# Performance work log

Measured on AMD Instinct MI355X. Metric: run time of the kernel, lower is better.

Reference implementation:

```python
import jax, jax.numpy as jnp
import numpy as np

HIDDEN = 4096
N_Q_HEADS = 32
N_KV_HEADS = 8
HEAD_DIM = 128
V_HEAD_DIM = 128
WINDOW = 1024
ROPE_THETA = 1000000.0
SEQ = 2048


def setup_inputs() -> dict:
    key = jax.random.key(0)
    ks = jax.random.split(key, 7)
    s = 0.02
    return {
        "hidden_states": jax.random.normal(ks[0], (SEQ, HIDDEN), dtype=jnp.float32),
        "positions": jnp.arange(SEQ, dtype=jnp.int32),
        "wq": jax.random.normal(ks[1], (HIDDEN, N_Q_HEADS * HEAD_DIM), dtype=jnp.float32) * s,
        "wk": jax.random.normal(ks[2], (HIDDEN, N_KV_HEADS * HEAD_DIM), dtype=jnp.float32) * s,
        "wv": jax.random.normal(ks[3], (HIDDEN, N_KV_HEADS * V_HEAD_DIM), dtype=jnp.float32) * s,
        "wo": jax.random.normal(ks[4], (N_Q_HEADS * V_HEAD_DIM, HIDDEN), dtype=jnp.float32) * s,
        "sink": jax.random.normal(ks[5], (N_Q_HEADS,), dtype=jnp.float32),
    }


def _apply_rope_neox(x, positions):
    # x: [S, H, D]; rotate full head_dim in neox (half-split) style
    d = x.shape[-1]
    inv_freq = 1.0 / (ROPE_THETA ** (jnp.arange(0, d, 2, dtype=jnp.float32) / d))
    freqs = positions.astype(jnp.float32)[:, None] * inv_freq[None, :]  # [S, D/2]
    cos = jnp.cos(freqs)[:, None, :]  # [S, 1, D/2]
    sin = jnp.sin(freqs)[:, None, :]
    x1, x2 = x[..., : d // 2], x[..., d // 2 :]
    return jnp.concatenate([x1 * cos - x2 * sin, x2 * cos + x1 * sin], axis=-1)


def reference(hidden_states, positions, wq, wk, wv, wo, sink):
    S = hidden_states.shape[0]
    scaling = HEAD_DIM ** -0.5
    q = (hidden_states @ wq).reshape(S, N_Q_HEADS, HEAD_DIM)
    k = (hidden_states @ wk).reshape(S, N_KV_HEADS, HEAD_DIM)
    v = (hidden_states @ wv).reshape(S, N_KV_HEADS, V_HEAD_DIM)

    q = _apply_rope_neox(q, positions)
    k = _apply_rope_neox(k, positions)

    groups = N_Q_HEADS // N_KV_HEADS
    k_rep = jnp.repeat(k, groups, axis=1)  # [S, Hq, D]
    v_rep = jnp.repeat(v, groups, axis=1)

    # [Hq, S(query), S(key)] attention scores
    scores = jnp.einsum("qhd,khd->hqk", q, k_rep) * scaling

    # causal + sliding-window mask: key j visible iff j <= i and i - j < WINDOW
    i = positions[:, None].astype(jnp.int32)
    j = positions[None, :].astype(jnp.int32)
    mask = (j <= i) & (i - j < WINDOW)  # [S, S]
    neg = jnp.finfo(scores.dtype).min
    scores = jnp.where(mask[None, :, :], scores, neg)

    # softmax with per-head attention sink logit in the denominator
    sink_l = sink[:, None, None]  # [Hq, 1, 1]
    m = jnp.maximum(scores.max(axis=-1, keepdims=True), sink_l)
    w = jnp.exp(scores - m)
    denom = w.sum(axis=-1, keepdims=True) + jnp.exp(sink_l - m)
    probs = w / denom

    attn = jnp.einsum("hqk,khd->qhd", probs, v_rep).reshape(S, N_Q_HEADS * V_HEAD_DIM)
    return attn @ wo
```

## Files before the change

kernel.cpp:

```cpp
#include <hip/hip_runtime.h>
#include <cstdint>
#include <cstddef>

typedef uint16_t u16;
typedef __bf16 bf16x8 __attribute__((ext_vector_type(8)));
typedef float f32x4 __attribute__((ext_vector_type(4)));
typedef u16 u16x8 __attribute__((ext_vector_type(8)));


__device__ __forceinline__ u16 f2bf(float f) {
    union { float f; uint32_t i; } v; v.f = f;
    uint32_t b = v.i;
    return (u16)((b + 0x7FFFu + ((b >> 16) & 1u)) >> 16);
}
__device__ __forceinline__ float bf2f(u16 u) {
    union { uint32_t i; float f; } v; v.i = ((uint32_t)u) << 16; return v.f;
}
__device__ __forceinline__ float nanfix(float x, float repl) {
    return (x == x && fabsf(x) < 1e30f) ? x : repl;
}
__device__ __forceinline__ void async16(const u16* g, u16* l) {
    __builtin_amdgcn_global_load_lds(
        (const __attribute__((address_space(1))) uint32_t*)g,
        (__attribute__((address_space(3))) uint32_t*)l, 16, 0, 0);
}

template<int N> __device__ __forceinline__ void waitvm() {
    static_assert(N >= 0 && N <= 14, "vmcnt range");
    if constexpr (N == 0)  asm volatile("s_waitcnt vmcnt(0)" ::: "memory");
    else if constexpr (N == 1)  asm volatile("s_waitcnt vmcnt(1)" ::: "memory");
    else if constexpr (N == 2)  asm volatile("s_waitcnt vmcnt(2)" ::: "memory");
    else if constexpr (N == 3)  asm volatile("s_waitcnt vmcnt(3)" ::: "memory");
    else if constexpr (N == 4)  asm volatile("s_waitcnt vmcnt(4)" ::: "memory");
    else if constexpr (N == 5)  asm volatile("s_waitcnt vmcnt(5)" ::: "memory");
    else if constexpr (N == 6)  asm volatile("s_waitcnt vmcnt(6)" ::: "memory");
    else if constexpr (N == 7)  asm volatile("s_waitcnt vmcnt(7)" ::: "memory");
    else if constexpr (N == 8)  asm volatile("s_waitcnt vmcnt(8)" ::: "memory");
    else if constexpr (N == 9)  asm volatile("s_waitcnt vmcnt(9)" ::: "memory");
    else if constexpr (N == 10) asm volatile("s_waitcnt vmcnt(10)" ::: "memory");
    else if constexpr (N == 11) asm volatile("s_waitcnt vmcnt(11)" ::: "memory");
    else if constexpr (N == 12) asm volatile("s_waitcnt vmcnt(12)" ::: "memory");
    else if constexpr (N == 13) asm volatile("s_waitcnt vmcnt(13)" ::: "memory");
    else                        asm volatile("s_waitcnt vmcnt(14)" ::: "memory");
}

__global__ void cvt_k(const float* __restrict__ in, u16* __restrict__ out) {
    const size_t i = ((size_t)blockIdx.x * 256 + threadIdx.x) * 8;
    const f32x4 a = *(const f32x4*)&in[i], b = *(const f32x4*)&in[i + 4];
    u16x8 s;
    #pragma unroll
    for (int e = 0; e < 4; e++) { s[e] = f2bf(a[e]); s[4 + e] = f2bf(b[e]); }
    *(u16x8*)&out[i] = s;
}

__global__ void cvtT_k(const float* __restrict__ in, u16* __restrict__ out,
                       int R, int C) {
    __shared__ float tile[64][65];
    const int bx = blockIdx.x * 64, by = blockIdx.y * 64;
    const int tid = threadIdx.x;
    const int lc = (tid & 15) * 4, lrw = tid >> 4;
    #pragma unroll
    for (int i = 0; i < 4; i++) {
        const f32x4 v = *(const f32x4*)&in[(size_t)(by + lrw + i * 16) * C + bx + lc];
        tile[lrw + i * 16][lc]     = v[0];
        tile[lrw + i * 16][lc + 1] = v[1];
        tile[lrw + i * 16][lc + 2] = v[2];
        tile[lrw + i * 16][lc + 3] = v[3];
    }
    __syncthreads();
    #pragma unroll
    for (int p = 0; p < 2; p++) {
        const int c = (tid >> 3) + p * 32, r0 = (tid & 7) * 8;
        u16x8 s;
        #pragma unroll
        for (int e = 0; e < 8; e++) s[e] = f2bf(tile[r0 + e][c]);
        *(u16x8*)&out[(size_t)(bx + c) * R + by + r0] = s;
    }
}


#define SB(g, kk, dst) async16(Bb + (size_t)((g) * 64 + rg) * 4096 + (kk) + sc, \
                               (dst) + ((g) * 64 + wave * 8) * 64)
#define SA(g, kk, dst) async16(Ab + (size_t)((g) * 32 + aro) * 4096 + (kk) + sc, \
                               (dst) + ((g) * 32 + wbA) * 64)

#define LOADA4(PH) do {                                                         \
    _Pragma("unroll")                                                           \
    for (int f = 0; f < 4; f++) {                                               \
        const int row = wr * 128 + ((PH) * 4 + f) * 16 + lr;                    \
        _Pragma("unroll")                                                       \
        for (int ks = 0; ks < 2; ks++)                                          \
            a[f][ks] = *(const bf16x8*)&Ac[row * 64 + (((ks * 4 + qd) ^ (row & 7)) * 8)]; \
    }                                                                           \
} while (0)

#define MFMAP4(PH) do {                                                         \
    __builtin_amdgcn_s_setprio(1);                                              \
    _Pragma("unroll")                                                           \
    for (int f = 0; f < 4; f++)                                                 \
        _Pragma("unroll")                                                       \
        for (int nn = 0; nn < NF; nn++)                                         \
            _Pragma("unroll")                                                   \
            for (int ks = 0; ks < 2; ks++)                                      \
                acc[(PH) * 4 + f][nn] = __builtin_amdgcn_mfma_f32_16x16x32_bf16(\
                    a[f][ks], b[nn][ks], acc[(PH) * 4 + f][nn], 0, 0, 0);       \
    __builtin_amdgcn_s_setprio(0);                                              \
} while (0)

#define PHASE_SYNC() do {                                                       \
    __builtin_amdgcn_s_barrier();                                               \
    asm volatile("s_waitcnt lgkmcnt(0)" ::: "memory");                          \
    __builtin_amdgcn_sched_barrier(0);                                          \
} while (0)

#define PHASE_END() do {                                                        \
    __builtin_amdgcn_s_barrier();                                               \
    __builtin_amdgcn_sched_barrier(0);                                          \
} while (0)

template<int NF, int ISS>
__device__ __forceinline__ void tile_body(
    const u16* __restrict__ Ab, const u16* __restrict__ Bb,
    const u16* Ac, const u16* Bc, u16* An, u16* Bn, int k1,
    int wave, int lr, int qd, int wr, int wc,
    int rg, int sc, int aro, int wbA, f32x4 (&acc)[8][NF])
{
    bf16x8 b[NF][2];
    bf16x8 a[4][2];

    #pragma unroll
    for (int nn = 0; nn < NF; nn++)
        #pragma unroll
        for (int ks = 0; ks < 2; ks++) {
            const int row = wc * (16 * NF) + nn * 16 + lr;
            b[nn][ks] = *(const bf16x8*)&Bc[row * 64 + (((ks * 4 + qd) ^ (row & 7)) * 8)];
        }
    LOADA4(0);
    if constexpr (ISS) {
        #pragma unroll
        for (int g = 0; g < NF; g++) SB(g, k1, Bn);
        SA(0, k1, An); SA(1, k1, An); SA(2, k1, An); SA(3, k1, An);
    }
    PHASE_SYNC();
    MFMAP4(0);
    waitvm<ISS ? NF + 4 : 0>();
    PHASE_END();
    LOADA4(1);
    PHASE_SYNC();
    MFMAP4(1);
    if constexpr (ISS) waitvm<2>();
    PHASE_END();
}

template<int NF, int MODE>
__global__ __launch_bounds__(512, 2) void gemm256(
    const u16* __restrict__ A, const u16* __restrict__ BT,
    u16* __restrict__ qk, u16* __restrict__ vT, float* __restrict__ Cf)
{
    alignas(16) __shared__ u16 As[2][256 * 64];
    alignas(16) __shared__ u16 Bs[2][NF * 64 * 64];

    const int tid = threadIdx.x;
    const int wave = tid >> 6, lane = tid & 63;
    const int lr = lane & 15, qd = lane >> 4;
    const int wr = wave >> 2, wc = wave & 3;

    const int x = blockIdx.x & 7, bi = blockIdx.x >> 3;
    const int m0 = ((x & 1) * 4 + (bi & 3)) * 256;
    const int n0 = ((x >> 1) * 8 + (bi >> 2)) * (NF * 64);

    const u16* __restrict__ Ab = A + (size_t)m0 * 4096;
    const u16* __restrict__ Bb = BT + (size_t)n0 * 4096;

    const int rg = tid >> 3;
    const int sc = ((tid & 7) ^ (rg & 7)) * 8;
    const int aro = (rg < 32) ? rg : (96 + rg);
    const int wbA = (wave < 4) ? wave * 8 : (96 + wave * 8);

    f32x4 acc[8][NF];
    #pragma unroll
    for (int i = 0; i < 8; i++)
        #pragma unroll
        for (int j = 0; j < NF; j++) acc[i][j] = (f32x4){0.f, 0.f, 0.f, 0.f};

    #pragma unroll
    for (int g = 0; g < NF; g++) SB(g, 0, &Bs[0][0]);
    SA(0, 0, &As[0][0]); SA(1, 0, &As[0][0]); SA(2, 0, &As[0][0]); SA(3, 0, &As[0][0]);
    waitvm<2>();
    __builtin_amdgcn_s_barrier();
    __builtin_amdgcn_sched_barrier(0);

    for (int t = 0; t < 63; ++t) {
        const bool odd = t & 1;
        tile_body<NF, 1>(Ab, Bb,
                         odd ? &As[1][0] : &As[0][0], odd ? &Bs[1][0] : &Bs[0][0],
                         odd ? &As[0][0] : &As[1][0], odd ? &Bs[0][0] : &Bs[1][0],
                         (t + 1) * 64, wave, lr, qd, wr, wc, rg, sc, aro, wbA, acc);
    }
    tile_body<NF, 0>(Ab, Bb, &As[1][0], &Bs[1][0], &As[0][0], &Bs[0][0], 0,
                     wave, lr, qd, wr, wc, rg, sc, aro, wbA, acc);

    #pragma unroll
    for (int i = 0; i < 8; i++)
        #pragma unroll
        for (int j = 0; j < NF; j++) {
            const int col = n0 + wc * (16 * NF) + j * 16 + lr;
            #pragma unroll
            for (int r = 0; r < 4; r++) {
                const int row = m0 + wr * 128 + i * 16 + qd * 4 + r;
                if constexpr (MODE == 0) {
                    const u16 val = f2bf(nanfix(acc[i][j][r], 1000.0f));
                    if (col < 5120) qk[(size_t)row * 5120 + col] = val;
                    else            vT[(size_t)(col - 5120) * 2048 + row] = val;
                } else {
                    Cf[(size_t)row * 4096 + col] = nanfix(acc[i][j][r], 30000.0f);
                }
            }
        }
}

#undef SB
#undef SA
#undef LOADA4
#undef MFMAP4
#undef PHASE_SYNC
#undef PHASE_END

__global__ void rope_k(u16* __restrict__ qk, const int* __restrict__ positions) {
    const int s = blockIdx.x;
    const int h = blockIdx.y * 4 + (threadIdx.x >> 6);
    const int t = threadIdx.x & 63;
    u16* base = qk + (size_t)s * 5120 + ((h < 32) ? h * 128 : 4096 + (h - 32) * 128);
    const float pos = (float)positions[s];
    const float freq = pos * exp2f(-(float)t * (19.931568569324174f / 64.f));
    const float c = cosf(freq), sn = sinf(freq);
    const float x1 = bf2f(base[t]), x2 = bf2f(base[t + 64]);
    base[t]      = f2bf(x1 * c - x2 * sn);
    base[t + 64] = f2bf(x2 * c + x1 * sn);
}

__global__ __launch_bounds__(256) void attn_k(
    const u16* __restrict__ qk, const u16* __restrict__ vT,
    const float* __restrict__ sink, u16* __restrict__ out)
{
    alignas(16) __shared__ u16 Ks[64 * 128];
    alignas(16) __shared__ u16 VsT[128 * 72];
    alignas(16) __shared__ u16 Ps[4][16 * 72];

    const int h = blockIdx.y, hk = h >> 2;
    const int q0 = blockIdx.x * 64;
    const int tid = threadIdx.x, wave = tid >> 6, lane = tid & 63;
    const int lr = lane & 15, qd = lane >> 4;
    const float scaling = 0.08838834764831845f;

    bf16x8 aq[4];
    #pragma unroll
    for (int kc = 0; kc < 4; kc++)
        aq[kc] = *(const bf16x8*)&qk[(size_t)(q0 + wave * 16 + lr) * 5120 + h * 128 + kc * 32 + qd * 8];

    const float sinkv = sink[h];
    float m_run[4], l_run[4];
    #pragma unroll
    for (int r = 0; r < 4; r++) { m_run[r] = sinkv; l_run[r] = 0.f; }
    f32x4 acc_o[8];
    #pragma unroll
    for (int i = 0; i < 8; i++) acc_o[i] = (f32x4){0.f, 0.f, 0.f, 0.f};

    const int jlo = (q0 - 1023) > 0 ? (q0 - 1023) : 0;
    const int t0 = jlo >> 6, t1 = q0 >> 6;

    for (int kt = t0; kt <= t1; kt++) {
        const int j0 = kt * 64;
        __syncthreads();
        #pragma unroll
        for (int p = 0; p < 4; p++) {
            const int idx = p * 256 + tid;
            const int r = idx >> 4, cs = idx & 15, c = cs ^ (r & 15);
            async16(&qk[(size_t)(j0 + r) * 5120 + 4096 + hk * 128 + c * 8],
                    Ks + (p * 256 + wave * 64) * 8);
        }
        #pragma unroll
        for (int p = 0; p < 4; p++) {
            const int idx = p * 256 + tid;
            const int vd = idx >> 3, sc2 = (idx & 7) * 8;
            const u16x8 v = *(const u16x8*)&vT[(size_t)(hk * 128 + vd) * 2048 + j0 + sc2];
            *(u16x8*)&VsT[vd * 72 + sc2] = v;
        }
        __syncthreads();

        float sv[4][4];
        #pragma unroll
        for (int nt = 0; nt < 4; nt++) {
            f32x4 s = (f32x4){0.f, 0.f, 0.f, 0.f};
            #pragma unroll
            for (int kc = 0; kc < 4; kc++) {
                const int krow = nt * 16 + lr;
                const bf16x8 bk = *(const bf16x8*)&Ks[(krow * 16 + ((kc * 4 + qd) ^ lr)) * 8];
                s = __builtin_amdgcn_mfma_f32_16x16x32_bf16(aq[kc], bk, s, 0, 0, 0);
            }
            #pragma unroll
            for (int r = 0; r < 4; r++) sv[nt][r] = s[r];
        }

        float rmax[4] = {-1e30f, -1e30f, -1e30f, -1e30f};
        #pragma unroll
        for (int nt = 0; nt < 4; nt++) {
            const int kpos = j0 + nt * 16 + lr;
            #pragma unroll
            for (int r = 0; r < 4; r++) {
                const int qpos = q0 + wave * 16 + qd * 4 + r;
                const bool ok = (kpos <= qpos) && (qpos - kpos < 1024);
                const float x = ok ? sv[nt][r] * scaling : -1e30f;
                sv[nt][r] = x;
                rmax[r] = fmaxf(rmax[r], x);
            }
        }
        #pragma unroll
        for (int off = 1; off < 16; off <<= 1)
            #pragma unroll
            for (int r = 0; r < 4; r++)
                rmax[r] = fmaxf(rmax[r], __shfl_xor(rmax[r], off, 64));

        float alpha[4], rsum[4];
        #pragma unroll
        for (int r = 0; r < 4; r++) {
            const float mnew = fmaxf(m_run[r], rmax[r]);
            alpha[r] = __expf(m_run[r] - mnew);
            m_run[r] = mnew;
            rsum[r] = 0.f;
        }
        #pragma unroll
        for (int nt = 0; nt < 4; nt++)
            #pragma unroll
            for (int r = 0; r < 4; r++) {
                const float p = __expf(sv[nt][r] - m_run[r]);
                sv[nt][r] = p;
                rsum[r] += p;
            }
        #pragma unroll
        for (int off = 1; off < 16; off <<= 1)
            #pragma unroll
            for (int r = 0; r < 4; r++)
                rsum[r] += __shfl_xor(rsum[r], off, 64);
        #pragma unroll
        for (int r = 0; r < 4; r++)
            l_run[r] = l_run[r] * alpha[r] + rsum[r];

        #pragma unroll
        for (int nt = 0; nt < 4; nt++)
            #pragma unroll
            for (int r = 0; r < 4; r++)
                Ps[wave][(qd * 4 + r) * 72 + nt * 16 + lr] = f2bf(sv[nt][r]);

        #pragma unroll
        for (int i = 0; i < 8; i++)
            #pragma unroll
            for (int r = 0; r < 4; r++) acc_o[i][r] *= alpha[r];

        asm volatile("s_waitcnt lgkmcnt(0)" ::: "memory");
        __builtin_amdgcn_sched_barrier(0);

        bf16x8 pa[2];
        #pragma unroll
        for (int kc = 0; kc < 2; kc++)
            pa[kc] = *(const bf16x8*)&Ps[wave][lr * 72 + kc * 32 + qd * 8];

        #pragma unroll
        for (int nt = 0; nt < 8; nt++)
            #pragma unroll
            for (int kc = 0; kc < 2; kc++) {
                const bf16x8 bv = *(const bf16x8*)&VsT[(nt * 16 + lr) * 72 + kc * 32 + qd * 8];
                acc_o[nt] = __builtin_amdgcn_mfma_f32_16x16x32_bf16(pa[kc], bv, acc_o[nt], 0, 0, 0);
            }
    }

    float invd[4];
    #pragma unroll
    for (int r = 0; r < 4; r++)
        invd[r] = 1.f / (l_run[r] + __expf(sinkv - m_run[r]));
    #pragma unroll
    for (int nt = 0; nt < 8; nt++) {
        const int col = h * 128 + nt * 16 + lr;
        #pragma unroll
        for (int r = 0; r < 4; r++) {
            const int row = q0 + wave * 16 + qd * 4 + r;
            out[(size_t)row * 4096 + col] = f2bf(nanfix(acc_o[nt][r] * invd[r], 8.0f));
        }
    }
}

extern "C" void kernel_launch(void* const* d_in, const int* in_sizes, int n_in,
                              void* d_out, int out_size, void* d_ws, size_t ws_size,
                              hipStream_t stream)
{
    (void)in_sizes; (void)n_in; (void)out_size; (void)ws_size;
    const float* hidden    = (const float*)d_in[0];
    const int*   positions = (const int*)d_in[1];
    const float* wq   = (const float*)d_in[2];
    const float* wk   = (const float*)d_in[3];
    const float* wv   = (const float*)d_in[4];
    const float* wo   = (const float*)d_in[5];
    const float* sink = (const float*)d_in[6];
    float* out = (float*)d_out;

    char* ws = (char*)d_ws;
    u16* hiddenB = (u16*)(ws);
    u16* wqkvT   = (u16*)(ws + (size_t)16777216);
    u16* qk      = (u16*)(ws + (size_t)67108864);
    u16* vT      = (u16*)(ws + (size_t)88080384);
    u16* woT     = (u16*)(ws);
    u16* attnB   = (u16*)(ws + (size_t)33554432);

    cvt_k <<<4096, 256, 0, stream>>>(hidden, hiddenB);
    cvtT_k<<<dim3(64, 64), 256, 0, stream>>>(wq, wqkvT, 4096, 4096);
    cvtT_k<<<dim3(16, 64), 256, 0, stream>>>(wk, wqkvT + (size_t)4096 * 4096, 4096, 1024);
    cvtT_k<<<dim3(16, 64), 256, 0, stream>>>(wv, wqkvT + (size_t)5120 * 4096, 4096, 1024);

    gemm256<3, 0><<<256, 512, 0, stream>>>(hiddenB, wqkvT, qk, vT, nullptr);

    cvtT_k<<<dim3(64, 64), 256, 0, stream>>>(wo, woT, 4096, 4096);

    rope_k<<<dim3(2048, 10), 256, 0, stream>>>(qk, positions);
    attn_k<<<dim3(32, 32), 256, 0, stream>>>(qk, vT, sink, attnB);

    gemm256<2, 1><<<256, 512, 0, stream>>>(attnB, woT, nullptr, nullptr, out);
}
```

Before: 512.3 us.

## Shrink GEMM tiles to 128-row blocks with 256 threads and more workgroups

Both bf16 GEMMs move from a 256-row, 512-thread tile (2x4 wave grid) to a 128-row, 256-thread tile in which each of 4 waves covers all rows and its own column slice. Block counts go from 256 to 768 for QKV and 512 for the output projection, and the block-index swizzle is reworked. The aim is better CU occupancy and load balance across the 256 CUs, since the old grid had only 256 blocks. In exchange, each block reuses loaded data less, so global and L2 traffic per FLOP rises.

New measurement: 507.5 us. About the same (-0.9%).

```diff
diff --git a/kernel.cpp b/kernel.cpp
--- a/kernel.cpp
+++ b/kernel.cpp
@@ -79,15 +79,15 @@
 }
 
 
-#define SB(g, kk, dst) async16(Bb + (size_t)((g) * 64 + rg) * 4096 + (kk) + sc, \
-                               (dst) + ((g) * 64 + wave * 8) * 64)
-#define SA(g, kk, dst) async16(Ab + (size_t)((g) * 32 + aro) * 4096 + (kk) + sc, \
-                               (dst) + ((g) * 32 + wbA) * 64)
+#define SB(g, kk, dst) async16(Bb + (size_t)((g) * 32 + rg) * 4096 + (kk) + sc, \
+                               (dst) + ((g) * 32 + wave * 8) * 64)
+#define SA(g, kk, dst) async16(Ab + (size_t)((g) * 32 + rg) * 4096 + (kk) + sc, \
+                               (dst) + ((g) * 32 + wave * 8) * 64)
 
 #define LOADA4(PH) do {                                                         \
     _Pragma("unroll")                                                           \
     for (int f = 0; f < 4; f++) {                                               \
-        const int row = wr * 128 + ((PH) * 4 + f) * 16 + lr;                    \
+        const int row = ((PH) * 4 + f) * 16 + lr;                               \
         _Pragma("unroll")                                                       \
         for (int ks = 0; ks < 2; ks++)                                          \
             a[f][ks] = *(const bf16x8*)&Ac[row * 64 + (((ks * 4 + qd) ^ (row & 7)) * 8)]; \
@@ -122,8 +122,8 @@
 __device__ __forceinline__ void tile_body(
     const u16* __restrict__ Ab, const u16* __restrict__ Bb,
     const u16* Ac, const u16* Bc, u16* An, u16* Bn, int k1,
-    int wave, int lr, int qd, int wr, int wc,
-    int rg, int sc, int aro, int wbA, f32x4 (&acc)[8][NF])
+    int wave, int lr, int qd, int wc,
+    int rg, int sc, f32x4 (&acc)[8][NF])
 {
     bf16x8 b[NF][2];
     bf16x8 a[4][2];
@@ -138,12 +138,12 @@
     LOADA4(0);
     if constexpr (ISS) {
         #pragma unroll
-        for (int g = 0; g < NF; g++) SB(g, k1, Bn);
+        for (int g = 0; g < 2 * NF; g++) SB(g, k1, Bn);
         SA(0, k1, An); SA(1, k1, An); SA(2, k1, An); SA(3, k1, An);
     }
     PHASE_SYNC();
     MFMAP4(0);
-    waitvm<ISS ? NF + 4 : 0>();
+    waitvm<ISS ? 2 * NF + 4 : 0>();
     PHASE_END();
     LOADA4(1);
     PHASE_SYNC();
@@ -153,29 +153,30 @@
 }
 
 template<int NF, int MODE>
-__global__ __launch_bounds__(512, 2) void gemm256(
+__global__ __launch_bounds__(256, 2) void gemm256(
     const u16* __restrict__ A, const u16* __restrict__ BT,
     u16* __restrict__ qk, u16* __restrict__ vT, float* __restrict__ Cf)
 {
-    alignas(16) __shared__ u16 As[2][256 * 64];
+    alignas(16) __shared__ u16 As[2][128 * 64];
     alignas(16) __shared__ u16 Bs[2][NF * 64 * 64];
+
+    constexpr int NTN = (MODE == 0) ? 48 : 32;
 
     const int tid = threadIdx.x;
     const int wave = tid >> 6, lane = tid & 63;
     const int lr = lane & 15, qd = lane >> 4;
-    const int wr = wave >> 2, wc = wave & 3;
+    const int wc = wave;
 
     const int x = blockIdx.x & 7, bi = blockIdx.x >> 3;
-    const int m0 = ((x & 1) * 4 + (bi & 3)) * 256;
-    const int n0 = ((x >> 1) * 8 + (bi >> 2)) * (NF * 64);
+    const int mi = (x & 3) * 4 + (bi & 3);
+    const int ni = (x >> 2) * (NTN / 2) + (bi >> 2);
+    const int m0 = mi * 128, n0 = ni * (NF * 64);
 
     const u16* __restrict__ Ab = A + (size_t)m0 * 4096;
     const u16* __restrict__ Bb = BT + (size_t)n0 * 4096;
 
     const int rg = tid >> 3;
     const int sc = ((tid & 7) ^ (rg & 7)) * 8;
-    const int aro = (rg < 32) ? rg : (96 + rg);
-    const int wbA = (wave < 4) ? wave * 8 : (96 + wave * 8);
 
     f32x4 acc[8][NF];
     #pragma unroll
@@ -184,7 +185,7 @@
         for (int j = 0; j < NF; j++) acc[i][j] = (f32x4){0.f, 0.f, 0.f, 0.f};
 
     #pragma unroll
-    for (int g = 0; g < NF; g++) SB(g, 0, &Bs[0][0]);
+    for (int g = 0; g < 2 * NF; g++) SB(g, 0, &Bs[0][0]);
     SA(0, 0, &As[0][0]); SA(1, 0, &As[0][0]); SA(2, 0, &As[0][0]); SA(3, 0, &As[0][0]);
     waitvm<2>();
     __builtin_amdgcn_s_barrier();
@@ -195,10 +196,10 @@
         tile_body<NF, 1>(Ab, Bb,
                          odd ? &As[1][0] : &As[0][0], odd ? &Bs[1][0] : &Bs[0][0],
                          odd ? &As[0][0] : &As[1][0], odd ? &Bs[0][0] : &Bs[1][0],
-                         (t + 1) * 64, wave, lr, qd, wr, wc, rg, sc, aro, wbA, acc);
+                         (t + 1) * 64, wave, lr, qd, wc, rg, sc, acc);
     }
     tile_body<NF, 0>(Ab, Bb, &As[1][0], &Bs[1][0], &As[0][0], &Bs[0][0], 0,
-                     wave, lr, qd, wr, wc, rg, sc, aro, wbA, acc);
+                     wave, lr, qd, wc, rg, sc, acc);
 
     #pragma unroll
     for (int i = 0; i < 8; i++)
@@ -207,7 +208,7 @@
             const int col = n0 + wc * (16 * NF) + j * 16 + lr;
             #pragma unroll
             for (int r = 0; r < 4; r++) {
-                const int row = m0 + wr * 128 + i * 16 + qd * 4 + r;
+                const int row = m0 + i * 16 + qd * 4 + r;
                 if constexpr (MODE == 0) {
                     const u16 val = f2bf(nanfix(acc[i][j][r], 1000.0f));
                     if (col < 5120) qk[(size_t)row * 5120 + col] = val;
@@ -416,12 +417,12 @@
     cvtT_k<<<dim3(16, 64), 256, 0, stream>>>(wk, wqkvT + (size_t)4096 * 4096, 4096, 1024);
     cvtT_k<<<dim3(16, 64), 256, 0, stream>>>(wv, wqkvT + (size_t)5120 * 4096, 4096, 1024);
 
-    gemm256<3, 0><<<256, 512, 0, stream>>>(hiddenB, wqkvT, qk, vT, nullptr);
+    gemm256<2, 0><<<768, 256, 0, stream>>>(hiddenB, wqkvT, qk, vT, nullptr);
 
     cvtT_k<<<dim3(64, 64), 256, 0, stream>>>(wo, woT, 4096, 4096);
 
     rope_k<<<dim3(2048, 10), 256, 0, stream>>>(qk, positions);
     attn_k<<<dim3(32, 32), 256, 0, stream>>>(qk, vT, sink, attnB);
 
-    gemm256<2, 1><<<256, 512, 0, stream>>>(attnB, woT, nullptr, nullptr, out);
-}
+    gemm256<2, 1><<<512, 256, 0, stream>>>(attnB, woT, nullptr, nullptr, out);
+}
```
